# Optimization experiments

Measured on AMD Instinct MI355X. Metric: run time of the kernel, lower is better.

The kernel has to match this reference:

```python
import itertools
import jax, jax.numpy as jnp
import numpy as np

NUM_GROUPS = 2  # num_squeeze_group
LN_EPS = 1e-6


def setup_inputs() -> dict:
    key = jax.random.key(0)
    ks = jax.random.split(key, 8)
    B, F, D = 1024, 32, 64
    P = F * (F - 1) // 2  # 496 pairs
    OUT = 512
    g = NUM_GROUPS
    red = max(1, F * g * 2 // 4)  # reduction_ratio = 4 -> 32
    emb_size = F * D
    return {
        "x": jax.random.normal(ks[0], (B, F, D), jnp.float32),
        "W1": jax.random.normal(ks[1], (F * 2 * g, red), jnp.float32) * (1.0 / np.sqrt(F * 2 * g)),
        "b1": jnp.zeros((red,), jnp.float32),
        "W2": jax.random.normal(ks[2], (red, emb_size), jnp.float32) * (1.0 / np.sqrt(red)),
        "b2": jnp.zeros((emb_size,), jnp.float32),
        "ln_scale": jnp.ones((emb_size,), jnp.float32),
        "ln_bias": jnp.zeros((emb_size,), jnp.float32),
        "Wp": jax.random.normal(ks[3], (P, D, D), jnp.float32) * (1.0 / np.sqrt(D)),
        "bp": jnp.zeros((P, D), jnp.float32),
        "Wo": jax.random.normal(ks[4], (P, OUT), jnp.float32) * (1.0 / np.sqrt(P)),
        "bo": jnp.zeros((OUT,), jnp.float32),
    }


def _pair_indices(F):
    pairs = np.array(list(itertools.combinations(range(F), 2)), dtype=np.int32)
    return pairs[:, 0], pairs[:, 1]


def reference(x, W1, b1, W2, b2, ln_scale, ln_bias, Wp, bp, Wo, bo):
    B, F, D = x.shape
    g = NUM_GROUPS

    # ---- SENet ----
    xg = x.reshape(B, F, g, D // g)
    # per-field [max(g), mean(g)], concatenated over fields -> [B, F*2g]
    z = jnp.concatenate([xg.max(axis=-1), xg.mean(axis=-1)], axis=-1).reshape(B, F * 2 * g)
    a1 = jax.nn.relu(z @ W1 + b1)            # [B, red]
    weights = a1 @ W2 + b2                   # [B, F*D]
    flat = x.reshape(B, F * D)
    senet = flat * weights + flat            # skip connection
    # layer norm over last axis
    mu = senet.mean(axis=-1, keepdims=True)
    var = senet.var(axis=-1, keepdims=True)
    senet = (senet - mu) * jax.lax.rsqrt(var + LN_EPS) * ln_scale + ln_bias

    # ---- BiLinear ('interaction', use_plus=True) ----
    i_idx, j_idx = _pair_indices(F)
    xi = x[:, i_idx, :]                      # [B, P, D]
    xj = x[:, j_idx, :]                      # [B, P, D]
    proj = jnp.einsum('bpd,pde->bpe', xi, Wp) + bp  # per-pair Dense(D->D)
    dots = jnp.sum(proj * xj, axis=-1)       # [B, P] batched dot (bi-linear+)
    bilinear = dots @ Wo + bo                # [B, OUT]

    return jnp.concatenate([senet, bilinear], axis=-1)
```

## Files before the change

kernel.cpp:

```cpp
#include <hip/hip_runtime.h>
#include <hip/hip_bf16.h>

#define F_FEAT 32
#define D_DIM 64
#define B_SZ 1024
#define EMB 2048
#define P_PAIRS 496
#define KPAD 512
#define OUT_N 512
#define OUT_STRIDE 2560
#define LN_EPS 1e-6f

typedef __attribute__((ext_vector_type(8))) short bf16x8;
typedef __attribute__((ext_vector_type(4))) float f32x4;

__device__ inline ushort f2bf(float f) {
    union { float f; unsigned u; } a; a.f = f;
    unsigned u = a.u;
    unsigned r = (u + 0x7FFFu + ((u >> 16) & 1u)) >> 16;
    return (ushort)r;
}
__device__ inline float bf2f(ushort u) {
    union { unsigned u; float f; } a; a.u = ((unsigned)u) << 16;
    return a.f;
}

__global__ __launch_bounds__(256) void k_prep(
        const float* __restrict__ Wp, ushort* __restrict__ Wpt,
        const float* __restrict__ Wo, ushort* __restrict__ Wot,
        ushort* __restrict__ db) {
    __shared__ float tile[64][65];
    int t = threadIdx.x;
    int blk = blockIdx.x;

    if (blk < 496) {
        int p = blk;
        const float* src = Wp + (size_t)p * 4096;
        ushort* dst = Wpt + (size_t)p * 4096;
#pragma unroll
        for (int it = 0; it < 4; ++it) {
            int d = it * 16 + (t >> 4);
            int e4 = (t & 15) * 4;
            float4 v = *reinterpret_cast<const float4*>(src + d * 64 + e4);
            tile[d][e4] = v.x; tile[d][e4 + 1] = v.y; tile[d][e4 + 2] = v.z; tile[d][e4 + 3] = v.w;
        }
        __syncthreads();
#pragma unroll
        for (int it = 0; it < 4; ++it) {
            int e = it * 16 + (t >> 4);
            int d4 = (t & 15) * 4;
            ushort4 o;
            o.x = f2bf(tile[d4][e]);     o.y = f2bf(tile[d4 + 1][e]);
            o.z = f2bf(tile[d4 + 2][e]); o.w = f2bf(tile[d4 + 3][e]);
            *reinterpret_cast<ushort4*>(dst + e * 64 + d4) = o;
        }
    } else if (blk < 560) {
        int bidx = blk - 496;
        int k0 = (bidx & 7) * 64;
        int n0 = (bidx >> 3) * 64;
#pragma unroll
        for (int it = 0; it < 4; ++it) {
            int kr = it * 16 + (t >> 4);
            int nc = (t & 15) * 4;
            int k = k0 + kr;
            float4 v = {0.f, 0.f, 0.f, 0.f};
            if (k < P_PAIRS) v = *reinterpret_cast<const float4*>(Wo + (size_t)k * OUT_N + n0 + nc);
            tile[kr][nc] = v.x; tile[kr][nc + 1] = v.y; tile[kr][nc + 2] = v.z; tile[kr][nc + 3] = v.w;
        }
        __syncthreads();
#pragma unroll
        for (int it = 0; it < 4; ++it) {
            int nr = it * 16 + (t >> 4);
            int kc = (t & 15) * 4;
            ushort4 o;
            o.x = f2bf(tile[kc][nr]);     o.y = f2bf(tile[kc + 1][nr]);
            o.z = f2bf(tile[kc + 2][nr]); o.w = f2bf(tile[kc + 3][nr]);
            *reinterpret_cast<ushort4*>(Wot + (size_t)(n0 + nr) * KPAD + k0 + kc) = o;
        }
    } else {
        int tid = (blk - 560) * 256 + t;
        if (tid < B_SZ) {
            bf16x8 z = {0, 0, 0, 0, 0, 0, 0, 0};
            ushort* dstp = db + (size_t)tid * KPAD + P_PAIRS;
            *reinterpret_cast<bf16x8*>(dstp) = z;
            *reinterpret_cast<bf16x8*>(dstp + 8) = z;
        }
    }
}

__global__ __launch_bounds__(512) void k_senet(
        const float* __restrict__ x, ushort* __restrict__ xb,
        const float* __restrict__ W1, const float* __restrict__ b1,
        const float* __restrict__ W2, const float* __restrict__ b2,
        const float* __restrict__ ln_s, const float* __restrict__ ln_b,
        float* __restrict__ out) {
    __shared__ float xs[4][EMB];
    __shared__ float zs[4][128];
    __shared__ float a1s[4][32];
    __shared__ float red[2][4][8];
    __shared__ float mlpred[2][128];
    int t = threadIdx.x;
    int b0 = blockIdx.x * 4;

    for (int r = 0; r < 4; ++r) {
        const float4* src = reinterpret_cast<const float4*>(x + (size_t)(b0 + r) * EMB);
        float4 v = src[t];
        reinterpret_cast<float4*>(&xs[r][0])[t] = v;
        ushort4 o;
        o.x = f2bf(v.x); o.y = f2bf(v.y); o.z = f2bf(v.z); o.w = f2bf(v.w);
        *reinterpret_cast<ushort4*>(xb + (size_t)(b0 + r) * EMB + t * 4) = o;
    }
    __syncthreads();

    {
        int g2 = t >> 1, sub = t & 1;
        int r = g2 >> 6, fg = g2 & 63, f = fg >> 1, gg = fg & 1;
        const float* base = &xs[r][f * 64 + gg * 32 + sub * 16];
        float mx = -INFINITY, sm = 0.f;
#pragma unroll
        for (int q = 0; q < 16; ++q) {
            float v = base[(q + t) & 15];
            mx = fmaxf(mx, v); sm += v;
        }
        float mx2 = __shfl_xor(mx, 1);
        float sm2 = __shfl_xor(sm, 1);
        mx = fmaxf(mx, mx2); sm += sm2;
        if (sub == 0) {
            zs[r][f * 4 + gg]     = mx;
            zs[r][f * 4 + 2 + gg] = sm * (1.f / 32.f);
        }
    }
    __syncthreads();

    if (t < 256) {
        int chunk = t >> 7, c = t & 127;
        int r = c >> 5, cc = c & 31;
        float acc = 0.f;
        int k0 = chunk * 64;
#pragma unroll
        for (int k = 0; k < 64; ++k) acc += zs[r][k0 + k] * W1[(k0 + k) * 32 + cc];
        mlpred[chunk][c] = acc;
    }
    __syncthreads();
    if (t < 128) {
        int r = t >> 5, cc = t & 31;
        a1s[r][cc] = fmaxf(mlpred[0][t] + mlpred[1][t] + b1[cc], 0.f);
    }
    __syncthreads();

    float acc[4][4];
#pragma unroll
    for (int r = 0; r < 4; ++r)
#pragma unroll
        for (int u = 0; u < 4; ++u) acc[r][u] = 0.f;

    for (int k = 0; k < 32; ++k) {
        float a0 = a1s[0][k], a1v = a1s[1][k], a2 = a1s[2][k], a3 = a1s[3][k];
#pragma unroll
        for (int u = 0; u < 4; ++u) {
            float wv = W2[k * EMB + t + 512 * u];
            acc[0][u] += a0 * wv; acc[1][u] += a1v * wv;
            acc[2][u] += a2 * wv; acc[3][u] += a3 * wv;
        }
    }
    float ssum[4], ssq[4];
#pragma unroll
    for (int r = 0; r < 4; ++r) { ssum[r] = 0.f; ssq[r] = 0.f; }
#pragma unroll
    for (int r = 0; r < 4; ++r) {
#pragma unroll
        for (int u = 0; u < 4; ++u) {
            int e = t + 512 * u;
            float w = acc[r][u] + b2[e];
            float s = xs[r][e] * (w + 1.0f);
            xs[r][e] = s;
            ssum[r] += s; ssq[r] += s * s;
        }
    }
    int lane = t & 63, w = t >> 6;
#pragma unroll
    for (int r = 0; r < 4; ++r) {
        float a = ssum[r], q = ssq[r];
        for (int off = 32; off; off >>= 1) { a += __shfl_down(a, off); q += __shfl_down(q, off); }
        if (lane == 0) { red[0][r][w] = a; red[1][r][w] = q; }
    }
    __syncthreads();
    float mu[4], rs[4];
#pragma unroll
    for (int r = 0; r < 4; ++r) {
        float a = 0.f, q = 0.f;
#pragma unroll
        for (int i = 0; i < 8; ++i) { a += red[0][r][i]; q += red[1][r][i]; }
        mu[r] = a * (1.f / 2048.f);
        float var = q * (1.f / 2048.f) - mu[r] * mu[r];
        rs[r] = rsqrtf(var + LN_EPS);
    }
#pragma unroll
    for (int r = 0; r < 4; ++r) {
#pragma unroll
        for (int u = 0; u < 4; ++u) {
            int e = t + 512 * u;
            float s = xs[r][e];
            out[(size_t)(b0 + r) * OUT_STRIDE + e] = (s - mu[r]) * rs[r] * ln_s[e] + ln_b[e];
        }
    }
}

__global__ __launch_bounds__(256) void k_dots(
        const ushort* __restrict__ xb, const ushort* __restrict__ Wpt,
        const float* __restrict__ bp, ushort* __restrict__ db) {
    int p = blockIdx.x >> 1;
    int h = blockIdx.x & 1;
    int i = 0, rem = p;
    while (rem >= F_FEAT - 1 - i) { rem -= F_FEAT - 1 - i; ++i; }
    int j = i + 1 + rem;

    int wave = threadIdx.x >> 6, lane = threadIdx.x & 63;
    int row = lane & 15, kg = lane >> 4;

    bf16x8 wfr[4][2];
#pragma unroll
    for (int nt = 0; nt < 4; ++nt)
#pragma unroll
        for (int ks = 0; ks < 2; ++ks)
            wfr[nt][ks] = *reinterpret_cast<const bf16x8*>(
                Wpt + (size_t)p * 4096 + (nt * 16 + row) * 64 + ks * 32 + kg * 8);

    f32x4 bb[4];
#pragma unroll
    for (int nt = 0; nt < 4; ++nt)
        bb[nt] = *reinterpret_cast<const f32x4*>(bp + p * 64 + nt * 16 + kg * 4);

    const ushort* xi_base = xb + (size_t)row * EMB + i * 64 + kg * 8;
    const ushort* xj_base = xb + (size_t)row * EMB + j * 64 + kg * 4;

    bf16x8 xifr[2][2];
    ushort4 xjw[2][4];

    auto loadit = [&](int it, int buf) {
        size_t boff = (size_t)(h * 512 + (wave * 8 + it) * 16) * EMB;
#pragma unroll
        for (int ks = 0; ks < 2; ++ks)
            xifr[buf][ks] = *reinterpret_cast<const bf16x8*>(xi_base + boff + ks * 32);
#pragma unroll
        for (int nt = 0; nt < 4; ++nt)
            xjw[buf][nt] = *reinterpret_cast<const ushort4*>(xj_base + boff + nt * 16);
    };

    loadit(0, 0);
#pragma unroll
    for (int it = 0; it < 8; ++it) {
        int cur = it & 1;
        if (it < 7) loadit(it + 1, cur ^ 1);

        f32x4 acc[4];
#pragma unroll
        for (int nt = 0; nt < 4; ++nt) {
            acc[nt] = bb[nt];
            acc[nt] = __builtin_amdgcn_mfma_f32_16x16x32_bf16(wfr[nt][0], xifr[cur][0], acc[nt], 0, 0, 0);
            acc[nt] = __builtin_amdgcn_mfma_f32_16x16x32_bf16(wfr[nt][1], xifr[cur][1], acc[nt], 0, 0, 0);
        }

        float v = 0.f;
#pragma unroll
        for (int nt = 0; nt < 4; ++nt) {
            v += acc[nt][0] * bf2f(xjw[cur][nt].x);
            v += acc[nt][1] * bf2f(xjw[cur][nt].y);
            v += acc[nt][2] * bf2f(xjw[cur][nt].z);
            v += acc[nt][3] * bf2f(xjw[cur][nt].w);
        }
        v += __shfl_xor(v, 16);
        v += __shfl_xor(v, 32);
        if (lane < 16) {
            int b0 = h * 512 + (wave * 8 + it) * 16;
            db[(size_t)(b0 + lane) * KPAD + p] = f2bf(v);
        }
    }
}

__global__ __launch_bounds__(256) void k_bilin2(
        const ushort* __restrict__ db, const ushort* __restrict__ Wot,
        const float* __restrict__ bo, float* __restrict__ out) {
    int mt  = blockIdx.x >> 4;
    int nt0 = blockIdx.x & 15;
    int wave = threadIdx.x >> 6, lane = threadIdx.x & 63;
    int row = lane & 15, kg = lane >> 4;
    int m0 = mt * 64 + wave * 16;
    int n0 = nt0 * 32;

    f32x4 acc0 = {0.f, 0.f, 0.f, 0.f};
    f32x4 acc1 = {0.f, 0.f, 0.f, 0.f};
    const ushort* arow  = db  + (size_t)(m0 + row) * KPAD + kg * 8;
    const ushort* brow0 = Wot + (size_t)(n0 + row) * KPAD + kg * 8;
    const ushort* brow1 = brow0 + 16 * KPAD;
#pragma unroll
    for (int ks = 0; ks < 16; ++ks) {
        bf16x8 a  = *reinterpret_cast<const bf16x8*>(arow  + ks * 32);
        bf16x8 b0 = *reinterpret_cast<const bf16x8*>(brow0 + ks * 32);
        bf16x8 b1 = *reinterpret_cast<const bf16x8*>(brow1 + ks * 32);
        acc0 = __builtin_amdgcn_mfma_f32_16x16x32_bf16(a, b0, acc0, 0, 0, 0);
        acc1 = __builtin_amdgcn_mfma_f32_16x16x32_bf16(a, b1, acc1, 0, 0, 0);
    }
    int col = row;
    float bo0 = bo[n0 + col], bo1 = bo[n0 + 16 + col];
#pragma unroll
    for (int r = 0; r < 4; ++r) {
        size_t orow = (size_t)(m0 + kg * 4 + r) * OUT_STRIDE + 2048 + n0;
        out[orow + col]      = acc0[r] + bo0;
        out[orow + 16 + col] = acc1[r] + bo1;
    }
}

extern "C" void kernel_launch(void* const* d_in, const int* in_sizes, int n_in,
                              void* d_out, int out_size, void* d_ws, size_t ws_size,
                              hipStream_t stream) {
    const float* x    = (const float*)d_in[0];
    const float* W1   = (const float*)d_in[1];
    const float* b1   = (const float*)d_in[2];
    const float* W2   = (const float*)d_in[3];
    const float* b2   = (const float*)d_in[4];
    const float* ln_s = (const float*)d_in[5];
    const float* ln_b = (const float*)d_in[6];
    const float* Wp   = (const float*)d_in[7];
    const float* bp   = (const float*)d_in[8];
    const float* Wo   = (const float*)d_in[9];
    const float* bo   = (const float*)d_in[10];
    float* out = (float*)d_out;

    ushort* xb   = (ushort*)d_ws;
    ushort* wpt  = (ushort*)((char*)d_ws + 4194304);
    ushort* db   = (ushort*)((char*)d_ws + 4194304 + 4063232);
    ushort* wot  = (ushort*)((char*)d_ws + 4194304 + 4063232 + 1048576);

    k_prep<<<568, 256, 0, stream>>>(Wp, wpt, Wo, wot, db);
    k_senet<<<B_SZ / 4, 512, 0, stream>>>(x, xb, W1, b1, W2, b2, ln_s, ln_b, out);
    k_dots<<<P_PAIRS * 2, 256, 0, stream>>>(xb, wpt, bp, db);
    k_bilin2<<<256, 256, 0, stream>>>(db, wot, bo, out);
}
```

Measured before the change: 57.30 us.

## Fuse all stages into one persistent kernel with grid-wide barriers

Merges the prep, SENet, pairwise-dot and output-GEMM kernels into a single 1024-block kernel that synchronises between stages with software global barriers built on atomic counters. The SENet stage is also reworked so each thread keeps 8 contiguous elements in registers instead of staging rows through shared memory. The goal is to remove multiple kernel launch gaps and tail effects, and to let independent weight prep run alongside SENet. The cost is two grid barriers that need all blocks co-resident, an extra memset launch, and a deadlock risk if occupancy assumptions fail. A fallback to the old four-kernel path is kept.

Measured after the change: 59.23 us. 1.03x slower.

```diff
diff --git a/kernel.cpp b/kernel.cpp
--- a/kernel.cpp
+++ b/kernel.cpp
@@ -10,6 +10,7 @@
 #define OUT_N 512
 #define OUT_STRIDE 2560
 #define LN_EPS 1e-6f
+#define NB 1024
 
 typedef __attribute__((ext_vector_type(8))) short bf16x8;
 typedef __attribute__((ext_vector_type(4))) float f32x4;
@@ -23,6 +24,315 @@
 __device__ inline float bf2f(ushort u) {
     union { unsigned u; float f; } a; a.u = ((unsigned)u) << 16;
     return a.f;
+}
+
+__device__ inline void gbarrier(unsigned* cnt, unsigned* flag) {
+    __syncthreads();
+    if (threadIdx.x == 0) {
+        __threadfence();
+        unsigned old = atomicAdd(cnt, 1u);
+        if (old == NB - 1u) {
+            __hip_atomic_store(flag, 1u, __ATOMIC_RELEASE, __HIP_MEMORY_SCOPE_AGENT);
+        } else {
+            while (__hip_atomic_load(flag, __ATOMIC_RELAXED, __HIP_MEMORY_SCOPE_AGENT) == 0u)
+                __builtin_amdgcn_s_sleep(8);
+        }
+        __threadfence();
+    }
+    __syncthreads();
+}
+
+__device__ inline void dots_vb(int vb, const ushort* __restrict__ xb,
+                               const ushort* __restrict__ Wpt,
+                               const float* __restrict__ bp,
+                               ushort* __restrict__ db) {
+    int p = vb >> 1;
+    int h = vb & 1;
+    int i = 0, rem = p;
+    while (rem >= F_FEAT - 1 - i) { rem -= F_FEAT - 1 - i; ++i; }
+    int j = i + 1 + rem;
+
+    int wave = threadIdx.x >> 6, lane = threadIdx.x & 63;
+    int row = lane & 15, kg = lane >> 4;
+
+    bf16x8 wfr[4][2];
+#pragma unroll
+    for (int nt = 0; nt < 4; ++nt)
+#pragma unroll
+        for (int ks = 0; ks < 2; ++ks)
+            wfr[nt][ks] = *reinterpret_cast<const bf16x8*>(
+                Wpt + (size_t)p * 4096 + (nt * 16 + row) * 64 + ks * 32 + kg * 8);
+
+    f32x4 bb[4];
+#pragma unroll
+    for (int nt = 0; nt < 4; ++nt)
+        bb[nt] = *reinterpret_cast<const f32x4*>(bp + p * 64 + nt * 16 + kg * 4);
+
+    const ushort* xi_base = xb + (size_t)row * EMB + i * 64 + kg * 8;
+    const ushort* xj_base = xb + (size_t)row * EMB + j * 64 + kg * 4;
+
+    bf16x8 xifr[2][2];
+    ushort4 xjw[2][4];
+
+    auto loadit = [&](int it, int buf) {
+        size_t boff = (size_t)(h * 512 + (wave * 8 + it) * 16) * EMB;
+#pragma unroll
+        for (int ks = 0; ks < 2; ++ks)
+            xifr[buf][ks] = *reinterpret_cast<const bf16x8*>(xi_base + boff + ks * 32);
+#pragma unroll
+        for (int nt = 0; nt < 4; ++nt)
+            xjw[buf][nt] = *reinterpret_cast<const ushort4*>(xj_base + boff + nt * 16);
+    };
+
+    loadit(0, 0);
+#pragma unroll
+    for (int it = 0; it < 8; ++it) {
+        int cur = it & 1;
+        if (it < 7) loadit(it + 1, cur ^ 1);
+
+        f32x4 acc[4];
+#pragma unroll
+        for (int nt = 0; nt < 4; ++nt) {
+            acc[nt] = bb[nt];
+            acc[nt] = __builtin_amdgcn_mfma_f32_16x16x32_bf16(wfr[nt][0], xifr[cur][0], acc[nt], 0, 0, 0);
+            acc[nt] = __builtin_amdgcn_mfma_f32_16x16x32_bf16(wfr[nt][1], xifr[cur][1], acc[nt], 0, 0, 0);
+        }
+
+        float v = 0.f;
+#pragma unroll
+        for (int nt = 0; nt < 4; ++nt) {
+            v += acc[nt][0] * bf2f(xjw[cur][nt].x);
+            v += acc[nt][1] * bf2f(xjw[cur][nt].y);
+            v += acc[nt][2] * bf2f(xjw[cur][nt].z);
+            v += acc[nt][3] * bf2f(xjw[cur][nt].w);
+        }
+        v += __shfl_xor(v, 16);
+        v += __shfl_xor(v, 32);
+        if (lane < 16) {
+            int b0 = h * 512 + (wave * 8 + it) * 16;
+            db[(size_t)(b0 + lane) * KPAD + p] = f2bf(v);
+        }
+    }
+}
+
+__device__ inline void bilin_vb(int vb, const ushort* __restrict__ db,
+                                const ushort* __restrict__ Wot,
+                                const float* __restrict__ bo,
+                                float* __restrict__ out) {
+    int mt  = vb >> 4;
+    int nt0 = vb & 15;
+    int wave = threadIdx.x >> 6, lane = threadIdx.x & 63;
+    int row = lane & 15, kg = lane >> 4;
+    int m0 = mt * 64 + wave * 16;
+    int n0 = nt0 * 32;
+
+    f32x4 acc0 = {0.f, 0.f, 0.f, 0.f};
+    f32x4 acc1 = {0.f, 0.f, 0.f, 0.f};
+    const ushort* arow  = db  + (size_t)(m0 + row) * KPAD + kg * 8;
+    const ushort* brow0 = Wot + (size_t)(n0 + row) * KPAD + kg * 8;
+    const ushort* brow1 = brow0 + 16 * KPAD;
+#pragma unroll
+    for (int ks = 0; ks < 16; ++ks) {
+        bf16x8 a  = *reinterpret_cast<const bf16x8*>(arow  + ks * 32);
+        bf16x8 b0 = *reinterpret_cast<const bf16x8*>(brow0 + ks * 32);
+        bf16x8 b1 = *reinterpret_cast<const bf16x8*>(brow1 + ks * 32);
+        acc0 = __builtin_amdgcn_mfma_f32_16x16x32_bf16(a, b0, acc0, 0, 0, 0);
+        acc1 = __builtin_amdgcn_mfma_f32_16x16x32_bf16(a, b1, acc1, 0, 0, 0);
+    }
+    int col = row;
+    float bo0 = bo[n0 + col], bo1 = bo[n0 + 16 + col];
+#pragma unroll
+    for (int r = 0; r < 4; ++r) {
+        size_t orow = (size_t)(m0 + kg * 4 + r) * OUT_STRIDE + 2048 + n0;
+        out[orow + col]      = acc0[r] + bo0;
+        out[orow + 16 + col] = acc1[r] + bo1;
+    }
+}
+
+__global__ __launch_bounds__(256, 4) void k_fused(
+        const float* __restrict__ x, ushort* __restrict__ xb,
+        const float* __restrict__ Wp, ushort* __restrict__ Wpt,
+        const float* __restrict__ Wo, ushort* __restrict__ Wot,
+        ushort* __restrict__ db,
+        const float* __restrict__ W1, const float* __restrict__ b1,
+        const float* __restrict__ W2, const float* __restrict__ b2,
+        const float* __restrict__ ln_s, const float* __restrict__ ln_b,
+        const float* __restrict__ bp, const float* __restrict__ bo,
+        float* __restrict__ out, unsigned* __restrict__ bar) {
+    __shared__ union {
+        float tile[64][65];
+        struct { float zs[4][128]; float a1s[4][32]; float red[2][4][4]; } sn;
+    } sm;
+    int t = threadIdx.x;
+    int blk = blockIdx.x;
+
+    if (blk < 256) {
+        int b0 = blk * 4;
+        int e0 = t * 8;
+        float xr[4][8];
+#pragma unroll
+        for (int r = 0; r < 4; ++r) {
+            const float* src = x + (size_t)(b0 + r) * EMB + e0;
+            float4 v0 = *reinterpret_cast<const float4*>(src);
+            float4 v1 = *reinterpret_cast<const float4*>(src + 4);
+            xr[r][0] = v0.x; xr[r][1] = v0.y; xr[r][2] = v0.z; xr[r][3] = v0.w;
+            xr[r][4] = v1.x; xr[r][5] = v1.y; xr[r][6] = v1.z; xr[r][7] = v1.w;
+            bf16x8 o;
+#pragma unroll
+            for (int u = 0; u < 8; ++u) o[u] = (short)f2bf(xr[r][u]);
+            *reinterpret_cast<bf16x8*>(xb + (size_t)(b0 + r) * EMB + e0) = o;
+        }
+        int f = t >> 3, gg = (t >> 2) & 1;
+#pragma unroll
+        for (int r = 0; r < 4; ++r) {
+            float mx = xr[r][0], sum = xr[r][0];
+#pragma unroll
+            for (int u = 1; u < 8; ++u) { mx = fmaxf(mx, xr[r][u]); sum += xr[r][u]; }
+            float m2 = __shfl_xor(mx, 1), s2 = __shfl_xor(sum, 1);
+            mx = fmaxf(mx, m2); sum += s2;
+            m2 = __shfl_xor(mx, 2); s2 = __shfl_xor(sum, 2);
+            mx = fmaxf(mx, m2); sum += s2;
+            if ((t & 3) == 0) {
+                sm.sn.zs[r][f * 4 + gg]     = mx;
+                sm.sn.zs[r][f * 4 + 2 + gg] = sum * (1.f / 32.f);
+            }
+        }
+        __syncthreads();
+        if (t < 128) {
+            int r = t >> 5, c = t & 31;
+            float acc = b1[c];
+            for (int k = 0; k < 128; ++k) acc += sm.sn.zs[r][k] * W1[k * 32 + c];
+            sm.sn.a1s[r][c] = fmaxf(acc, 0.f);
+        }
+        __syncthreads();
+        float acc[4][8];
+#pragma unroll
+        for (int r = 0; r < 4; ++r)
+#pragma unroll
+            for (int u = 0; u < 8; ++u) acc[r][u] = 0.f;
+        for (int k = 0; k < 32; ++k) {
+            float4 w0 = *reinterpret_cast<const float4*>(W2 + (size_t)k * EMB + e0);
+            float4 w1 = *reinterpret_cast<const float4*>(W2 + (size_t)k * EMB + e0 + 4);
+#pragma unroll
+            for (int r = 0; r < 4; ++r) {
+                float a = sm.sn.a1s[r][k];
+                acc[r][0] += a * w0.x; acc[r][1] += a * w0.y;
+                acc[r][2] += a * w0.z; acc[r][3] += a * w0.w;
+                acc[r][4] += a * w1.x; acc[r][5] += a * w1.y;
+                acc[r][6] += a * w1.z; acc[r][7] += a * w1.w;
+            }
+        }
+        float4 b2v0 = *reinterpret_cast<const float4*>(b2 + e0);
+        float4 b2v1 = *reinterpret_cast<const float4*>(b2 + e0 + 4);
+        float b2a[8] = {b2v0.x, b2v0.y, b2v0.z, b2v0.w, b2v1.x, b2v1.y, b2v1.z, b2v1.w};
+        float ssum[4], ssq[4];
+#pragma unroll
+        for (int r = 0; r < 4; ++r) {
+            ssum[r] = 0.f; ssq[r] = 0.f;
+#pragma unroll
+            for (int u = 0; u < 8; ++u) {
+                float w = acc[r][u] + b2a[u];
+                float s = xr[r][u] * (w + 1.0f);
+                xr[r][u] = s;
+                ssum[r] += s; ssq[r] += s * s;
+            }
+        }
+        int lane = t & 63, wv = t >> 6;
+#pragma unroll
+        for (int r = 0; r < 4; ++r) {
+            float a = ssum[r], q = ssq[r];
+            for (int off = 32; off; off >>= 1) { a += __shfl_down(a, off); q += __shfl_down(q, off); }
+            if (lane == 0) { sm.sn.red[0][r][wv] = a; sm.sn.red[1][r][wv] = q; }
+        }
+        __syncthreads();
+        float4 lsv0 = *reinterpret_cast<const float4*>(ln_s + e0);
+        float4 lsv1 = *reinterpret_cast<const float4*>(ln_s + e0 + 4);
+        float4 lbv0 = *reinterpret_cast<const float4*>(ln_b + e0);
+        float4 lbv1 = *reinterpret_cast<const float4*>(ln_b + e0 + 4);
+        float lsa[8] = {lsv0.x, lsv0.y, lsv0.z, lsv0.w, lsv1.x, lsv1.y, lsv1.z, lsv1.w};
+        float lba[8] = {lbv0.x, lbv0.y, lbv0.z, lbv0.w, lbv1.x, lbv1.y, lbv1.z, lbv1.w};
+#pragma unroll
+        for (int r = 0; r < 4; ++r) {
+            float a = 0.f, q = 0.f;
+#pragma unroll
+            for (int i = 0; i < 4; ++i) { a += sm.sn.red[0][r][i]; q += sm.sn.red[1][r][i]; }
+            float mu = a * (1.f / 2048.f);
+            float var = q * (1.f / 2048.f) - mu * mu;
+            float rs = rsqrtf(var + LN_EPS);
+            float* orow = out + (size_t)(b0 + r) * OUT_STRIDE + e0;
+            float4 o0, o1;
+            o0.x = (xr[r][0] - mu) * rs * lsa[0] + lba[0];
+            o0.y = (xr[r][1] - mu) * rs * lsa[1] + lba[1];
+            o0.z = (xr[r][2] - mu) * rs * lsa[2] + lba[2];
+            o0.w = (xr[r][3] - mu) * rs * lsa[3] + lba[3];
+            o1.x = (xr[r][4] - mu) * rs * lsa[4] + lba[4];
+            o1.y = (xr[r][5] - mu) * rs * lsa[5] + lba[5];
+            o1.z = (xr[r][6] - mu) * rs * lsa[6] + lba[6];
+            o1.w = (xr[r][7] - mu) * rs * lsa[7] + lba[7];
+            *reinterpret_cast<float4*>(orow)     = o0;
+            *reinterpret_cast<float4*>(orow + 4) = o1;
+        }
+    } else if (blk < 752) {
+        int p = blk - 256;
+        const float* src = Wp + (size_t)p * 4096;
+        ushort* dst = Wpt + (size_t)p * 4096;
+#pragma unroll
+        for (int it = 0; it < 4; ++it) {
+            int d = it * 16 + (t >> 4);
+            int e4 = (t & 15) * 4;
+            float4 v = *reinterpret_cast<const float4*>(src + d * 64 + e4);
+            sm.tile[d][e4] = v.x; sm.tile[d][e4 + 1] = v.y;
+            sm.tile[d][e4 + 2] = v.z; sm.tile[d][e4 + 3] = v.w;
+        }
+        __syncthreads();
+#pragma unroll
+        for (int it = 0; it < 4; ++it) {
+            int e = it * 16 + (t >> 4);
+            int d4 = (t & 15) * 4;
+            ushort4 o;
+            o.x = f2bf(sm.tile[d4][e]);     o.y = f2bf(sm.tile[d4 + 1][e]);
+            o.z = f2bf(sm.tile[d4 + 2][e]); o.w = f2bf(sm.tile[d4 + 3][e]);
+            *reinterpret_cast<ushort4*>(dst + e * 64 + d4) = o;
+        }
+    } else if (blk < 816) {
+        int bidx = blk - 752;
+        int k0 = (bidx & 7) * 64;
+        int n0 = (bidx >> 3) * 64;
+#pragma unroll
+        for (int it = 0; it < 4; ++it) {
+            int kr = it * 16 + (t >> 4);
+            int nc = (t & 15) * 4;
+            int k = k0 + kr;
+            float4 v = {0.f, 0.f, 0.f, 0.f};
+            if (k < P_PAIRS) v = *reinterpret_cast<const float4*>(Wo + (size_t)k * OUT_N + n0 + nc);
+            sm.tile[kr][nc] = v.x; sm.tile[kr][nc + 1] = v.y;
+            sm.tile[kr][nc + 2] = v.z; sm.tile[kr][nc + 3] = v.w;
+        }
+        __syncthreads();
+#pragma unroll
+        for (int it = 0; it < 4; ++it) {
+            int nr = it * 16 + (t >> 4);
+            int kc = (t & 15) * 4;
+            ushort4 o;
+            o.x = f2bf(sm.tile[kc][nr]);     o.y = f2bf(sm.tile[kc + 1][nr]);
+            o.z = f2bf(sm.tile[kc + 2][nr]); o.w = f2bf(sm.tile[kc + 3][nr]);
+            *reinterpret_cast<ushort4*>(Wot + (size_t)(n0 + nr) * KPAD + k0 + kc) = o;
+        }
+    } else if (blk < 820) {
+        int tid = (blk - 816) * 256 + t;
+        bf16x8 z = {0, 0, 0, 0, 0, 0, 0, 0};
+        ushort* dstp = db + (size_t)tid * KPAD + P_PAIRS;
+        *reinterpret_cast<bf16x8*>(dstp) = z;
+        *reinterpret_cast<bf16x8*>(dstp + 8) = z;
+    }
+
+    gbarrier(bar + 0, bar + 1);
+
+    if (blk < P_PAIRS * 2) dots_vb(blk, xb, Wpt, bp, db);
+
+    gbarrier(bar + 2, bar + 3);
+
+    if (blk < 256) bilin_vb(blk, db, Wot, bo, out);
 }
 
 __global__ __launch_bounds__(256) void k_prep(
@@ -98,7 +408,6 @@
     __shared__ float zs[4][128];
     __shared__ float a1s[4][32];
     __shared__ float red[2][4][8];
-    __shared__ float mlpred[2][128];
     int t = threadIdx.x;
     int b0 = blockIdx.x * 4;
 
@@ -112,39 +421,24 @@
     }
     __syncthreads();
 
-    {
-        int g2 = t >> 1, sub = t & 1;
-        int r = g2 >> 6, fg = g2 & 63, f = fg >> 1, gg = fg & 1;
-        const float* base = &xs[r][f * 64 + gg * 32 + sub * 16];
+    if (t < 256) {
+        int r = t >> 6, f = (t >> 1) & 31, gg = t & 1;
+        const float* base = &xs[r][f * 64 + gg * 32];
         float mx = -INFINITY, sm = 0.f;
-#pragma unroll
-        for (int q = 0; q < 16; ++q) {
-            float v = base[(q + t) & 15];
+        for (int q = 0; q < 32; ++q) {
+            float v = base[(q + t) & 31];
             mx = fmaxf(mx, v); sm += v;
         }
-        float mx2 = __shfl_xor(mx, 1);
-        float sm2 = __shfl_xor(sm, 1);
-        mx = fmaxf(mx, mx2); sm += sm2;
-        if (sub == 0) {
-            zs[r][f * 4 + gg]     = mx;
-            zs[r][f * 4 + 2 + gg] = sm * (1.f / 32.f);
-        }
+        zs[r][f * 4 + gg]     = mx;
+        zs[r][f * 4 + 2 + gg] = sm * (1.f / 32.f);
     }
     __syncthreads();
 
-    if (t < 256) {
-        int chunk = t >> 7, c = t & 127;
-        int r = c >> 5, cc = c & 31;
-        float acc = 0.f;
-        int k0 = chunk * 64;
-#pragma unroll
-        for (int k = 0; k < 64; ++k) acc += zs[r][k0 + k] * W1[(k0 + k) * 32 + cc];
-        mlpred[chunk][c] = acc;
-    }
-    __syncthreads();
     if (t < 128) {
-        int r = t >> 5, cc = t & 31;
-        a1s[r][cc] = fmaxf(mlpred[0][t] + mlpred[1][t] + b1[cc], 0.f);
+        int r = t >> 5, c = t & 31;
+        float acc = b1[c];
+        for (int k = 0; k < 128; ++k) acc += zs[r][k] * W1[k * 32 + c];
+        a1s[r][c] = fmaxf(acc, 0.f);
     }
     __syncthreads();
 
@@ -209,106 +503,13 @@
 __global__ __launch_bounds__(256) void k_dots(
         const ushort* __restrict__ xb, const ushort* __restrict__ Wpt,
         const float* __restrict__ bp, ushort* __restrict__ db) {
-    int p = blockIdx.x >> 1;
-    int h = blockIdx.x & 1;
-    int i = 0, rem = p;
-    while (rem >= F_FEAT - 1 - i) { rem -= F_FEAT - 1 - i; ++i; }
-    int j = i + 1 + rem;
-
-    int wave = threadIdx.x >> 6, lane = threadIdx.x & 63;
-    int row = lane & 15, kg = lane >> 4;
-
-    bf16x8 wfr[4][2];
-#pragma unroll
-    for (int nt = 0; nt < 4; ++nt)
-#pragma unroll
-        for (int ks = 0; ks < 2; ++ks)
-            wfr[nt][ks] = *reinterpret_cast<const bf16x8*>(
-                Wpt + (size_t)p * 4096 + (nt * 16 + row) * 64 + ks * 32 + kg * 8);
-
-    f32x4 bb[4];
-#pragma unroll
-    for (int nt = 0; nt < 4; ++nt)
-        bb[nt] = *reinterpret_cast<const f32x4*>(bp + p * 64 + nt * 16 + kg * 4);
-
-    const ushort* xi_base = xb + (size_t)row * EMB + i * 64 + kg * 8;
-    const ushort* xj_base = xb + (size_t)row * EMB + j * 64 + kg * 4;
-
-    bf16x8 xifr[2][2];
-    ushort4 xjw[2][4];
-
-    auto loadit = [&](int it, int buf) {
-        size_t boff = (size_t)(h * 512 + (wave * 8 + it) * 16) * EMB;
-#pragma unroll
-        for (int ks = 0; ks < 2; ++ks)
-            xifr[buf][ks] = *reinterpret_cast<const bf16x8*>(xi_base + boff + ks * 32);
-#pragma unroll
-        for (int nt = 0; nt < 4; ++nt)
-            xjw[buf][nt] = *reinterpret_cast<const ushort4*>(xj_base + boff + nt * 16);
-    };
-
-    loadit(0, 0);
-#pragma unroll
-    for (int it = 0; it < 8; ++it) {
-        int cur = it & 1;
-        if (it < 7) loadit(it + 1, cur ^ 1);
-
-        f32x4 acc[4];
-#pragma unroll
-        for (int nt = 0; nt < 4; ++nt) {
-            acc[nt] = bb[nt];
-            acc[nt] = __builtin_amdgcn_mfma_f32_16x16x32_bf16(wfr[nt][0], xifr[cur][0], acc[nt], 0, 0, 0);
-            acc[nt] = __builtin_amdgcn_mfma_f32_16x16x32_bf16(wfr[nt][1], xifr[cur][1], acc[nt], 0, 0, 0);
-        }
-
-        float v = 0.f;
-#pragma unroll
-        for (int nt = 0; nt < 4; ++nt) {
-            v += acc[nt][0] * bf2f(xjw[cur][nt].x);
-            v += acc[nt][1] * bf2f(xjw[cur][nt].y);
-            v += acc[nt][2] * bf2f(xjw[cur][nt].z);
-            v += acc[nt][3] * bf2f(xjw[cur][nt].w);
-        }
-        v += __shfl_xor(v, 16);
-        v += __shfl_xor(v, 32);
-        if (lane < 16) {
-            int b0 = h * 512 + (wave * 8 + it) * 16;
-            db[(size_t)(b0 + lane) * KPAD + p] = f2bf(v);
-        }
-    }
+    dots_vb(blockIdx.x, xb, Wpt, bp, db);
 }
 
 __global__ __launch_bounds__(256) void k_bilin2(
         const ushort* __restrict__ db, const ushort* __restrict__ Wot,
         const float* __restrict__ bo, float* __restrict__ out) {
-    int mt  = blockIdx.x >> 4;
-    int nt0 = blockIdx.x & 15;
-    int wave = threadIdx.x >> 6, lane = threadIdx.x & 63;
-    int row = lane & 15, kg = lane >> 4;
-    int m0 = mt * 64 + wave * 16;
-    int n0 = nt0 * 32;
-
-    f32x4 acc0 = {0.f, 0.f, 0.f, 0.f};
-    f32x4 acc1 = {0.f, 0.f, 0.f, 0.f};
-    const ushort* arow  = db  + (size_t)(m0 + row) * KPAD + kg * 8;
-    const ushort* brow0 = Wot + (size_t)(n0 + row) * KPAD + kg * 8;
-    const ushort* brow1 = brow0 + 16 * KPAD;
-#pragma unroll
-    for (int ks = 0; ks < 16; ++ks) {
-        bf16x8 a  = *reinterpret_cast<const bf16x8*>(arow  + ks * 32);
-        bf16x8 b0 = *reinterpret_cast<const bf16x8*>(brow0 + ks * 32);
-        bf16x8 b1 = *reinterpret_cast<const bf16x8*>(brow1 + ks * 32);
-        acc0 = __builtin_amdgcn_mfma_f32_16x16x32_bf16(a, b0, acc0, 0, 0, 0);
-        acc1 = __builtin_amdgcn_mfma_f32_16x16x32_bf16(a, b1, acc1, 0, 0, 0);
-    }
-    int col = row;
-    float bo0 = bo[n0 + col], bo1 = bo[n0 + 16 + col];
-#pragma unroll
-    for (int r = 0; r < 4; ++r) {
-        size_t orow = (size_t)(m0 + kg * 4 + r) * OUT_STRIDE + 2048 + n0;
-        out[orow + col]      = acc0[r] + bo0;
-        out[orow + 16 + col] = acc1[r] + bo1;
-    }
+    bilin_vb(blockIdx.x, db, Wot, bo, out);
 }
 
 extern "C" void kernel_launch(void* const* d_in, const int* in_sizes, int n_in,
@@ -331,9 +532,19 @@
     ushort* wpt  = (ushort*)((char*)d_ws + 4194304);
     ushort* db   = (ushort*)((char*)d_ws + 4194304 + 4063232);
     ushort* wot  = (ushort*)((char*)d_ws + 4194304 + 4063232 + 1048576);
-
-    k_prep<<<568, 256, 0, stream>>>(Wp, wpt, Wo, wot, db);
-    k_senet<<<B_SZ / 4, 512, 0, stream>>>(x, xb, W1, b1, W2, b2, ln_s, ln_b, out);
-    k_dots<<<P_PAIRS * 2, 256, 0, stream>>>(xb, wpt, bp, db);
-    k_bilin2<<<256, 256, 0, stream>>>(db, wot, bo, out);
-}
+    unsigned* bar = (unsigned*)((char*)d_ws + 9830400);
+
+    int maxblk = 0;
+    (void)hipOccupancyMaxActiveBlocksPerMultiprocessor(&maxblk, k_fused, 256, 0);
+
+    if (maxblk >= 4) {
+        hipMemsetAsync(bar, 0, 16, stream);
+        k_fused<<<NB, 256, 0, stream>>>(x, xb, Wp, wpt, Wo, wot, db,
+                                        W1, b1, W2, b2, ln_s, ln_b, bp, bo, out, bar);
+    } else {
+        k_prep<<<568, 256, 0, stream>>>(Wp, wpt, Wo, wot, db);
+        k_senet<<<B_SZ / 4, 512, 0, stream>>>(x, xb, W1, b1, W2, b2, ln_s, ln_b, out);
+        k_dots<<<P_PAIRS * 2, 256, 0, stream>>>(xb, wpt, bp, db);
+        k_bilin2<<<256, 256, 0, stream>>>(db, wot, bo, out);
+    }
+}
```

## Keep SENet rows in registers and vectorize W2/LN accesses; reorder dots block mapping

Applied to the files above, without the earlier changes.

k_senet no longer stages the four input rows in a 32KB shared-memory buffer. Each thread keeps its contiguous 4 elements per row in registers and computes the per-group max/mean with xor shuffles. The W2, b2, ln_scale, ln_bias loads and the output stores become float4-vectorized over contiguous elements, which cuts LDS traffic and raises occupancy. In k_dots, the block-to-(pair,half) mapping changes so consecutive blocks take different pairs for the same half, which alters weight cache locality across blocks.

Result: slower. 88.18 us (+53.9%).

```diff
diff --git a/kernel.cpp b/kernel.cpp
--- a/kernel.cpp
+++ b/kernel.cpp
@@ -94,40 +94,41 @@
         const float* __restrict__ W2, const float* __restrict__ b2,
         const float* __restrict__ ln_s, const float* __restrict__ ln_b,
         float* __restrict__ out) {
-    __shared__ float xs[4][EMB];
     __shared__ float zs[4][128];
     __shared__ float a1s[4][32];
+    __shared__ float mlpred[2][128];
     __shared__ float red[2][4][8];
-    __shared__ float mlpred[2][128];
     int t = threadIdx.x;
     int b0 = blockIdx.x * 4;
-
-    for (int r = 0; r < 4; ++r) {
-        const float4* src = reinterpret_cast<const float4*>(x + (size_t)(b0 + r) * EMB);
-        float4 v = src[t];
-        reinterpret_cast<float4*>(&xs[r][0])[t] = v;
+    int e0 = t * 4;
+
+    float xr[4][4];
+#pragma unroll
+    for (int r = 0; r < 4; ++r) {
+        float4 v = *reinterpret_cast<const float4*>(x + (size_t)(b0 + r) * EMB + e0);
+        xr[r][0] = v.x; xr[r][1] = v.y; xr[r][2] = v.z; xr[r][3] = v.w;
         ushort4 o;
         o.x = f2bf(v.x); o.y = f2bf(v.y); o.z = f2bf(v.z); o.w = f2bf(v.w);
-        *reinterpret_cast<ushort4*>(xb + (size_t)(b0 + r) * EMB + t * 4) = o;
-    }
-    __syncthreads();
+        *reinterpret_cast<ushort4*>(xb + (size_t)(b0 + r) * EMB + e0) = o;
+    }
 
     {
-        int g2 = t >> 1, sub = t & 1;
-        int r = g2 >> 6, fg = g2 & 63, f = fg >> 1, gg = fg & 1;
-        const float* base = &xs[r][f * 64 + gg * 32 + sub * 16];
-        float mx = -INFINITY, sm = 0.f;
-#pragma unroll
-        for (int q = 0; q < 16; ++q) {
-            float v = base[(q + t) & 15];
-            mx = fmaxf(mx, v); sm += v;
-        }
-        float mx2 = __shfl_xor(mx, 1);
-        float sm2 = __shfl_xor(sm, 1);
-        mx = fmaxf(mx, mx2); sm += sm2;
-        if (sub == 0) {
-            zs[r][f * 4 + gg]     = mx;
-            zs[r][f * 4 + 2 + gg] = sm * (1.f / 32.f);
+        int f = t >> 4, gg = (t >> 3) & 1;
+#pragma unroll
+        for (int r = 0; r < 4; ++r) {
+            float mx = xr[r][0], sum = xr[r][0];
+#pragma unroll
+            for (int u = 1; u < 4; ++u) { mx = fmaxf(mx, xr[r][u]); sum += xr[r][u]; }
+            float m2 = __shfl_xor(mx, 1), s2 = __shfl_xor(sum, 1);
+            mx = fmaxf(mx, m2); sum += s2;
+            m2 = __shfl_xor(mx, 2); s2 = __shfl_xor(sum, 2);
+            mx = fmaxf(mx, m2); sum += s2;
+            m2 = __shfl_xor(mx, 4); s2 = __shfl_xor(sum, 4);
+            mx = fmaxf(mx, m2); sum += s2;
+            if ((t & 7) == 0) {
+                zs[r][f * 4 + gg]     = mx;
+                zs[r][f * 4 + 2 + gg] = sum * (1.f / 32.f);
+            }
         }
     }
     __syncthreads();
@@ -148,69 +149,60 @@
     }
     __syncthreads();
 
-    float acc[4][4];
-#pragma unroll
-    for (int r = 0; r < 4; ++r)
-#pragma unroll
-        for (int u = 0; u < 4; ++u) acc[r][u] = 0.f;
-
+    f32x4 acc[4];
+#pragma unroll
+    for (int r = 0; r < 4; ++r) { f32x4 z = {0.f,0.f,0.f,0.f}; acc[r] = z; }
     for (int k = 0; k < 32; ++k) {
+        f32x4 w = *reinterpret_cast<const f32x4*>(W2 + (size_t)k * EMB + e0);
         float a0 = a1s[0][k], a1v = a1s[1][k], a2 = a1s[2][k], a3 = a1s[3][k];
+        acc[0] += a0 * w; acc[1] += a1v * w; acc[2] += a2 * w; acc[3] += a3 * w;
+    }
+    f32x4 b2v = *reinterpret_cast<const f32x4*>(b2 + e0);
+
+    float ssum[4], ssq[4];
+#pragma unroll
+    for (int r = 0; r < 4; ++r) {
+        ssum[r] = 0.f; ssq[r] = 0.f;
 #pragma unroll
         for (int u = 0; u < 4; ++u) {
-            float wv = W2[k * EMB + t + 512 * u];
-            acc[0][u] += a0 * wv; acc[1][u] += a1v * wv;
-            acc[2][u] += a2 * wv; acc[3][u] += a3 * wv;
-        }
-    }
-    float ssum[4], ssq[4];
-#pragma unroll
-    for (int r = 0; r < 4; ++r) { ssum[r] = 0.f; ssq[r] = 0.f; }
-#pragma unroll
-    for (int r = 0; r < 4; ++r) {
-#pragma unroll
-        for (int u = 0; u < 4; ++u) {
-            int e = t + 512 * u;
-            float w = acc[r][u] + b2[e];
-            float s = xs[r][e] * (w + 1.0f);
-            xs[r][e] = s;
+            float w = acc[r][u] + b2v[u];
+            float s = xr[r][u] * (w + 1.0f);
+            xr[r][u] = s;
             ssum[r] += s; ssq[r] += s * s;
         }
     }
-    int lane = t & 63, w = t >> 6;
+    int lane = t & 63, wv = t >> 6;
 #pragma unroll
     for (int r = 0; r < 4; ++r) {
         float a = ssum[r], q = ssq[r];
         for (int off = 32; off; off >>= 1) { a += __shfl_down(a, off); q += __shfl_down(q, off); }
-        if (lane == 0) { red[0][r][w] = a; red[1][r][w] = q; }
+        if (lane == 0) { red[0][r][wv] = a; red[1][r][wv] = q; }
     }
     __syncthreads();
-    float mu[4], rs[4];
+
+    f32x4 lsv = *reinterpret_cast<const f32x4*>(ln_s + e0);
+    f32x4 lbv = *reinterpret_cast<const f32x4*>(ln_b + e0);
 #pragma unroll
     for (int r = 0; r < 4; ++r) {
         float a = 0.f, q = 0.f;
 #pragma unroll
         for (int i = 0; i < 8; ++i) { a += red[0][r][i]; q += red[1][r][i]; }
-        mu[r] = a * (1.f / 2048.f);
-        float var = q * (1.f / 2048.f) - mu[r] * mu[r];
-        rs[r] = rsqrtf(var + LN_EPS);
-    }
-#pragma unroll
-    for (int r = 0; r < 4; ++r) {
-#pragma unroll
-        for (int u = 0; u < 4; ++u) {
-            int e = t + 512 * u;
-            float s = xs[r][e];
-            out[(size_t)(b0 + r) * OUT_STRIDE + e] = (s - mu[r]) * rs[r] * ln_s[e] + ln_b[e];
-        }
+        float mu = a * (1.f / 2048.f);
+        float var = q * (1.f / 2048.f) - mu * mu;
+        float rs = rsqrtf(var + LN_EPS);
+        f32x4 o;
+#pragma unroll
+        for (int u = 0; u < 4; ++u) o[u] = (xr[r][u] - mu) * rs * lsv[u] + lbv[u];
+        *reinterpret_cast<f32x4*>(out + (size_t)(b0 + r) * OUT_STRIDE + e0) = o;
     }
 }
 
 __global__ __launch_bounds__(256) void k_dots(
         const ushort* __restrict__ xb, const ushort* __restrict__ Wpt,
         const float* __restrict__ bp, ushort* __restrict__ db) {
-    int p = blockIdx.x >> 1;
-    int h = blockIdx.x & 1;
+    int blk = blockIdx.x;
+    int h = (blk >= P_PAIRS) ? 1 : 0;
+    int p = blk - h * P_PAIRS;
     int i = 0, rem = p;
     while (rem >= F_FEAT - 1 - i) { rem -= F_FEAT - 1 - i; ++i; }
     int j = i + 1 + rem;
```

## Split k_dots batch into quarters and split-K the bilinear output GEMM

Applied to the files above, without the earlier changes.

k_dots now launches four blocks per pair instead of two, each covering 256 batch rows with four iterations, and drops the manual double-buffered prefetch of x fragments. k_bilin2 goes to 512 threads, where two wave groups each handle half of K and the partial sums are combined through shared memory before the bias add and store. The goal is more parallelism and shorter dependency chains per wave on both kernels. The cost is reloading each pair's Wp fragments in twice as many blocks, the lost load/compute overlap in k_dots, and an extra barrier plus LDS round trip in k_bilin2.

Result: slower. 61.78 us (+7.8%).

```diff
diff --git a/kernel.cpp b/kernel.cpp
--- a/kernel.cpp
+++ b/kernel.cpp
@@ -209,8 +209,8 @@
 __global__ __launch_bounds__(256) void k_dots(
         const ushort* __restrict__ xb, const ushort* __restrict__ Wpt,
         const float* __restrict__ bp, ushort* __restrict__ db) {
-    int p = blockIdx.x >> 1;
-    int h = blockIdx.x & 1;
+    int p = blockIdx.x >> 2;
+    int q = blockIdx.x & 3;
     int i = 0, rem = p;
     while (rem >= F_FEAT - 1 - i) { rem -= F_FEAT - 1 - i; ++i; }
     int j = i + 1 + rem;
@@ -231,83 +231,90 @@
     for (int nt = 0; nt < 4; ++nt)
         bb[nt] = *reinterpret_cast<const f32x4*>(bp + p * 64 + nt * 16 + kg * 4);
 
-    const ushort* xi_base = xb + (size_t)row * EMB + i * 64 + kg * 8;
-    const ushort* xj_base = xb + (size_t)row * EMB + j * 64 + kg * 4;
-
-    bf16x8 xifr[2][2];
-    ushort4 xjw[2][4];
-
-    auto loadit = [&](int it, int buf) {
-        size_t boff = (size_t)(h * 512 + (wave * 8 + it) * 16) * EMB;
+#pragma unroll
+    for (int it = 0; it < 4; ++it) {
+        int b0 = q * 256 + (wave * 4 + it) * 16;
+
+        bf16x8 xifr[2];
 #pragma unroll
         for (int ks = 0; ks < 2; ++ks)
-            xifr[buf][ks] = *reinterpret_cast<const bf16x8*>(xi_base + boff + ks * 32);
+            xifr[ks] = *reinterpret_cast<const bf16x8*>(
+                xb + (size_t)(b0 + row) * EMB + i * 64 + ks * 32 + kg * 8);
+
+        ushort4 xjw[4];
 #pragma unroll
         for (int nt = 0; nt < 4; ++nt)
-            xjw[buf][nt] = *reinterpret_cast<const ushort4*>(xj_base + boff + nt * 16);
-    };
-
-    loadit(0, 0);
-#pragma unroll
-    for (int it = 0; it < 8; ++it) {
-        int cur = it & 1;
-        if (it < 7) loadit(it + 1, cur ^ 1);
+            xjw[nt] = *reinterpret_cast<const ushort4*>(
+                xb + (size_t)(b0 + row) * EMB + j * 64 + nt * 16 + kg * 4);
 
         f32x4 acc[4];
 #pragma unroll
         for (int nt = 0; nt < 4; ++nt) {
             acc[nt] = bb[nt];
-            acc[nt] = __builtin_amdgcn_mfma_f32_16x16x32_bf16(wfr[nt][0], xifr[cur][0], acc[nt], 0, 0, 0);
-            acc[nt] = __builtin_amdgcn_mfma_f32_16x16x32_bf16(wfr[nt][1], xifr[cur][1], acc[nt], 0, 0, 0);
+            acc[nt] = __builtin_amdgcn_mfma_f32_16x16x32_bf16(wfr[nt][0], xifr[0], acc[nt], 0, 0, 0);
+            acc[nt] = __builtin_amdgcn_mfma_f32_16x16x32_bf16(wfr[nt][1], xifr[1], acc[nt], 0, 0, 0);
         }
 
         float v = 0.f;
 #pragma unroll
         for (int nt = 0; nt < 4; ++nt) {
-            v += acc[nt][0] * bf2f(xjw[cur][nt].x);
-            v += acc[nt][1] * bf2f(xjw[cur][nt].y);
-            v += acc[nt][2] * bf2f(xjw[cur][nt].z);
-            v += acc[nt][3] * bf2f(xjw[cur][nt].w);
+            v += acc[nt][0] * bf2f(xjw[nt].x);
+            v += acc[nt][1] * bf2f(xjw[nt].y);
+            v += acc[nt][2] * bf2f(xjw[nt].z);
+            v += acc[nt][3] * bf2f(xjw[nt].w);
         }
         v += __shfl_xor(v, 16);
         v += __shfl_xor(v, 32);
-        if (lane < 16) {
-            int b0 = h * 512 + (wave * 8 + it) * 16;
+        if (lane < 16)
             db[(size_t)(b0 + lane) * KPAD + p] = f2bf(v);
-        }
-    }
-}
-
-__global__ __launch_bounds__(256) void k_bilin2(
+    }
+}
+
+__global__ __launch_bounds__(512) void k_bilin2(
         const ushort* __restrict__ db, const ushort* __restrict__ Wot,
         const float* __restrict__ bo, float* __restrict__ out) {
+    __shared__ float part[4][64][8];
+    int t = threadIdx.x;
     int mt  = blockIdx.x >> 4;
     int nt0 = blockIdx.x & 15;
-    int wave = threadIdx.x >> 6, lane = threadIdx.x & 63;
+    int wave = t >> 6, lane = t & 63;
+    int tile = wave & 3, khalf = wave >> 2;
     int row = lane & 15, kg = lane >> 4;
-    int m0 = mt * 64 + wave * 16;
+    int m0 = mt * 64 + tile * 16;
     int n0 = nt0 * 32;
 
     f32x4 acc0 = {0.f, 0.f, 0.f, 0.f};
     f32x4 acc1 = {0.f, 0.f, 0.f, 0.f};
-    const ushort* arow  = db  + (size_t)(m0 + row) * KPAD + kg * 8;
-    const ushort* brow0 = Wot + (size_t)(n0 + row) * KPAD + kg * 8;
+    const ushort* arow  = db  + (size_t)(m0 + row) * KPAD + khalf * 256 + kg * 8;
+    const ushort* brow0 = Wot + (size_t)(n0 + row) * KPAD + khalf * 256 + kg * 8;
     const ushort* brow1 = brow0 + 16 * KPAD;
 #pragma unroll
-    for (int ks = 0; ks < 16; ++ks) {
+    for (int ks = 0; ks < 8; ++ks) {
         bf16x8 a  = *reinterpret_cast<const bf16x8*>(arow  + ks * 32);
         bf16x8 b0 = *reinterpret_cast<const bf16x8*>(brow0 + ks * 32);
         bf16x8 b1 = *reinterpret_cast<const bf16x8*>(brow1 + ks * 32);
         acc0 = __builtin_amdgcn_mfma_f32_16x16x32_bf16(a, b0, acc0, 0, 0, 0);
         acc1 = __builtin_amdgcn_mfma_f32_16x16x32_bf16(a, b1, acc1, 0, 0, 0);
     }
-    int col = row;
-    float bo0 = bo[n0 + col], bo1 = bo[n0 + 16 + col];
-#pragma unroll
-    for (int r = 0; r < 4; ++r) {
-        size_t orow = (size_t)(m0 + kg * 4 + r) * OUT_STRIDE + 2048 + n0;
-        out[orow + col]      = acc0[r] + bo0;
-        out[orow + 16 + col] = acc1[r] + bo1;
+    if (khalf == 1) {
+#pragma unroll
+        for (int r = 0; r < 4; ++r) {
+            part[tile][lane][r]     = acc0[r];
+            part[tile][lane][r + 4] = acc1[r];
+        }
+    }
+    __syncthreads();
+    if (khalf == 0) {
+        int col = row;
+        float bo0 = bo[n0 + col], bo1 = bo[n0 + 16 + col];
+#pragma unroll
+        for (int r = 0; r < 4; ++r) {
+            float v0 = acc0[r] + part[tile][lane][r];
+            float v1 = acc1[r] + part[tile][lane][r + 4];
+            size_t orow = (size_t)(m0 + kg * 4 + r) * OUT_STRIDE + 2048 + n0;
+            out[orow + col]      = v0 + bo0;
+            out[orow + 16 + col] = v1 + bo1;
+        }
     }
 }
 
@@ -334,6 +341,6 @@
 
     k_prep<<<568, 256, 0, stream>>>(Wp, wpt, Wo, wot, db);
     k_senet<<<B_SZ / 4, 512, 0, stream>>>(x, xb, W1, b1, W2, b2, ln_s, ln_b, out);
-    k_dots<<<P_PAIRS * 2, 256, 0, stream>>>(xb, wpt, bp, db);
-    k_bilin2<<<256, 256, 0, stream>>>(db, wot, bo, out);
-}
+    k_dots<<<P_PAIRS * 4, 256, 0, stream>>>(xb, wpt, bp, db);
+    k_bilin2<<<256, 512, 0, stream>>>(db, wot, bo, out);
+}
```
